# Kernel optimization log

Measured on AMD Instinct MI355X. Metric: run time of the kernel, lower is better.

The kernel has to match this reference:

```python
import jax, jax.numpy as jnp
import numpy as np

B, H, W, C = 16, 56, 56, 512
NH = 16
WS = 7
SHIFT = 3
HIDDEN = int(C * 4.0)
N = WS * WS
EPS = 1e-5


def _window_partition(x):
    # x: [B, H, W, C] -> [B*nW, N, C]
    b, h, w, c = x.shape
    x = x.reshape(b, h // WS, WS, w // WS, WS, c).transpose(0, 1, 3, 2, 4, 5)
    return x.reshape(-1, N, c)


def _window_reverse(win, h, w):
    c = win.shape[-1]
    x = win.reshape(-1, h // WS, w // WS, WS, WS, c).transpose(0, 1, 3, 2, 4, 5)
    return x.reshape(-1, h, w, c)


def _layernorm(x, g, b):
    mu = jnp.mean(x, axis=-1, keepdims=True)
    var = jnp.mean(jnp.square(x - mu), axis=-1, keepdims=True)
    return (x - mu) * jax.lax.rsqrt(var + EPS) * g + b


def _make_rel_coords_table():
    ch = np.arange(-(WS - 1), WS)
    cw = np.arange(-(WS - 1), WS)
    t = np.expand_dims(np.transpose(np.stack(np.meshgrid(ch, cw, indexing='ij')), [1, 2, 0]), 0).astype(np.float64)
    t[..., 0] /= (WS - 1)
    t[..., 1] /= (WS - 1)
    t *= 8
    t = np.sign(t) * np.log2(np.abs(t) + 1.0) / np.log2(8)
    return jnp.asarray(t, jnp.float32)  # [1, 2WS-1, 2WS-1, 2]


def _make_rel_pos_index():
    ch = np.arange(WS)
    cw = np.arange(WS)
    coords = np.reshape(np.stack(np.meshgrid(ch, cw, indexing='ij')), [2, -1])
    rel = np.expand_dims(coords, -1) - np.expand_dims(coords, -2)
    rel = np.transpose(rel, [1, 2, 0])
    rel[..., 0] += WS - 1
    rel[..., 1] += WS - 1
    rel[..., 0] *= 2 * WS - 1
    return jnp.asarray(np.sum(rel, -1), jnp.int32)  # [N, N]


def _make_attn_mask():
    img = np.zeros((H, W), np.float32)
    cnt = 0
    for hs in (slice(0, -WS), slice(-WS, -SHIFT), slice(-SHIFT, None)):
        for ws_ in (slice(0, -WS), slice(-WS, -SHIFT), slice(-SHIFT, None)):
            img[hs, ws_] = cnt
            cnt += 1
    x = img.reshape(1, H // WS, WS, W // WS, WS, 1).transpose(0, 1, 3, 2, 4, 5).reshape(-1, N)
    diff = x[:, :, None] - x[:, None, :]
    return jnp.asarray(np.where(diff != 0, -100.0, 0.0).astype(np.float32))  # [nW, N, N]


def setup_inputs() -> dict:
    key = jax.random.key(0)
    ks = jax.random.split(key, 16)
    s = 0.02
    return {
        'x': jax.random.normal(ks[0], (B, H, W, C), jnp.float32),
        'qkv_w': jax.random.normal(ks[1], (C, 3 * C), jnp.float32) * s,
        'q_bias': jnp.zeros((C,), jnp.float32),
        'v_bias': jnp.zeros((C,), jnp.float32),
        'proj_w': jax.random.normal(ks[2], (C, C), jnp.float32) * s,
        'proj_b': jnp.zeros((C,), jnp.float32),
        'logit_scale': jnp.full((NH, 1, 1), np.log(10.0), jnp.float32),
        'cpb_w1': jax.random.normal(ks[3], (2, 512), jnp.float32) * s,
        'cpb_b1': jnp.zeros((512,), jnp.float32),
        'cpb_w2': jax.random.normal(ks[4], (512, NH), jnp.float32) * s,
        'rel_coords_table': _make_rel_coords_table(),
        'gamma1': jnp.ones((C,), jnp.float32),
        'beta1': jnp.zeros((C,), jnp.float32),
        'gamma2': jnp.ones((C,), jnp.float32),
        'beta2': jnp.zeros((C,), jnp.float32),
        'fc1_w': jax.random.normal(ks[5], (C, HIDDEN), jnp.float32) * s,
        'fc1_b': jnp.zeros((HIDDEN,), jnp.float32),
        'fc2_w': jax.random.normal(ks[6], (HIDDEN, C), jnp.float32) * s,
        'fc2_b': jnp.zeros((C,), jnp.float32),
        'rel_pos_index': _make_rel_pos_index(),
        'attn_mask': _make_attn_mask(),
    }


def _forward(x, qkv_w, q_bias, v_bias, proj_w, proj_b, logit_scale,
             cpb_w1, cpb_b1, cpb_w2, rel_coords_table,
             gamma1, beta1, gamma2, beta2, fc1_w, fc1_b, fc2_w, fc2_b,
             rel_pos_index, attn_mask):
    hd = C // NH
    shortcut = x
    # cyclic shift + window partition
    xs = jnp.roll(x, (-SHIFT, -SHIFT), axis=(1, 2))
    xw = _window_partition(xs)  # [B*nW, N, C]
    # qkv with (q, 0, v) bias
    qkv_bias = jnp.concatenate([q_bias, jnp.zeros_like(v_bias), v_bias], axis=0)
    qkv = xw @ qkv_w + qkv_bias
    qkv = qkv.reshape(-1, N, 3, NH, hd).transpose(2, 0, 3, 1, 4)
    q, k, v = qkv[0], qkv[1], qkv[2]  # [BW, NH, N, hd]
    # cosine attention with learned temperature
    qn = q / jnp.linalg.norm(q, axis=-1, keepdims=True)
    kn = k / jnp.linalg.norm(k, axis=-1, keepdims=True)
    scale = jnp.exp(jnp.minimum(logit_scale, jnp.log(100.0)))
    attn = jnp.einsum('bhnd,bhmd->bhnm', qn, kn) * scale
    # continuous position bias via small MLP + gather
    cpb = jax.nn.relu(rel_coords_table @ cpb_w1 + cpb_b1) @ cpb_w2  # [1,2W-1,2W-1,NH]
    table = cpb.reshape(-1, NH)
    bias = table[rel_pos_index.reshape(-1)].reshape(N, N, NH).transpose(2, 0, 1)
    bias = 16.0 * jax.nn.sigmoid(bias)
    attn = attn + bias[None]
    # shifted-window mask
    nW = attn_mask.shape[0]
    attn = attn.reshape(-1, nW, NH, N, N) + attn_mask[None, :, None]
    attn = jax.nn.softmax(attn.reshape(-1, NH, N, N), axis=-1)
    out = jnp.einsum('bhnm,bhmd->bhnd', attn, v).transpose(0, 2, 1, 3).reshape(-1, N, C)
    out = out @ proj_w + proj_b
    # reverse windows + reverse shift
    out = _window_reverse(out, H, W)
    out = jnp.roll(out, (SHIFT, SHIFT), axis=(1, 2))
    # Swin-V2 res-post-norm residual blocks
    x1 = shortcut + _layernorm(out, gamma1, beta1)
    h = jax.nn.gelu(x1 @ fc1_w + fc1_b, approximate=False) @ fc2_w + fc2_b
    return x1 + _layernorm(h, gamma2, beta2)


def reference(x, qkv_w, q_bias, v_bias, proj_w, proj_b, logit_scale,
              cpb_w1, cpb_b1, cpb_w2, rel_coords_table,
              gamma1, beta1, gamma2, beta2, fc1_w, fc1_b, fc2_w, fc2_b,
              rel_pos_index, attn_mask):
    return _forward(x, qkv_w, q_bias, v_bias, proj_w, proj_b, logit_scale,
                    cpb_w1, cpb_b1, cpb_w2, rel_coords_table,
                    gamma1, beta1, gamma2, beta2, fc1_w, fc1_b, fc2_w, fc2_b,
                    rel_pos_index, attn_mask)
```

## Files before the change

kernel.cpp:

```cpp
#include <hip/hip_runtime.h>
#include <hip/hip_bf16.h>
#include <cmath>

typedef __hip_bfloat16 bf16;
typedef __attribute__((ext_vector_type(8))) __bf16 bf16x8;
typedef __attribute__((ext_vector_type(4))) float f32x4;
typedef __attribute__((ext_vector_type(4))) short short4v;

#define NROWS 50176

static __device__ __forceinline__ float b2f(bf16 v) { return __bfloat162float(v); }
static __device__ __forceinline__ bf16 f2b(float v) { return __float2bfloat16(v); }

static __device__ __forceinline__ void gl16(const bf16* g, bf16* l) {
  __builtin_amdgcn_global_load_lds((const __attribute__((address_space(1))) void*)g,
                                   (__attribute__((address_space(3))) void*)l, 16, 0, 0);
}

static __device__ __forceinline__ size_t pix_base(int row) {
  if (row >= NROWS) row = NROWS - 1;
  int win = row / 49, tok = row - win * 49;
  int b = win >> 6, wi = win & 63;
  int th = tok / 7, tw = tok - th * 7;
  int h = (wi >> 3) * 7 + th + 3; if (h >= 56) h -= 56;
  int w = (wi & 7) * 7 + tw + 3;  if (w >= 56) w -= 56;
  return (((size_t)b * 56 + h) * 56 + w) * 512;
}

__global__ __launch_bounds__(256) void diag_fill(float* out, float val, int n) {
  int i = blockIdx.x * 256 + threadIdx.x;
  if (i < n) out[i] = val;
}

__global__ __launch_bounds__(256) void transpose_f2b(const float* __restrict__ in,
                                                     bf16* __restrict__ out,
                                                     int R, int C) {
  __shared__ float tile[32][33];
  int c0 = blockIdx.x * 32, r0 = blockIdx.y * 32;
  int tx = threadIdx.x & 31, ty = threadIdx.x >> 5;
  for (int i = ty; i < 32; i += 8)
    tile[i][tx] = in[(size_t)(r0 + i) * C + c0 + tx];
  __syncthreads();
  for (int i = ty; i < 32; i += 8)
    out[(size_t)(c0 + i) * R + r0 + tx] = f2b(tile[tx][i]);
}

__global__ __launch_bounds__(256) void conv_f2b(const float* __restrict__ in,
                                                bf16* __restrict__ outb, int n8) {
  for (int i = blockIdx.x * 256 + threadIdx.x; i < n8; i += gridDim.x * 256) {
    float4 u0 = *(const float4*)&in[(size_t)i * 8];
    float4 u1 = *(const float4*)&in[(size_t)i * 8 + 4];
    bf16 h8[8] = {f2b(u0.x), f2b(u0.y), f2b(u0.z), f2b(u0.w),
                  f2b(u1.x), f2b(u1.y), f2b(u1.z), f2b(u1.w)};
    *(uint4*)&outb[(size_t)i * 8] = *(uint4*)h8;
  }
}

__global__ void prep_small(const float* qb, const float* vb, const float* pb,
                           const float* f1b, const float* f2b_, const float* ls,
                           float* qkvb, float* pbf, float* f1bf, float* f2bf,
                           float* scale) {
  int tid = blockIdx.x * 256 + threadIdx.x;
  if (tid < 512)       qkvb[tid] = qb[tid];
  else if (tid < 1024) qkvb[tid] = 0.f;
  else if (tid < 1536) qkvb[tid] = vb[tid - 1024];
  if (tid < 512)  pbf[tid]  = pb[tid];
  if (tid < 2048) f1bf[tid] = f1b[tid];
  if (tid < 512)  f2bf[tid] = f2b_[tid];
  if (tid < 16)   scale[tid] = expf(fminf(ls[tid], 4.6051701859880914f));
}

__global__ __launch_bounds__(256) void prep_cpb(const float* __restrict__ coords,
                                                const float* __restrict__ w1,
                                                const float* __restrict__ b1,
                                                const float* __restrict__ w2,
                                                float* __restrict__ table) {
  __shared__ float hid[512];
  __shared__ float part[256];
  int idx = blockIdx.x;
  float c0 = coords[idx * 2], c1 = coords[idx * 2 + 1];
  int tid = threadIdx.x;
  for (int h = tid; h < 512; h += 256) {
    float v = c0 * w1[h] + c1 * w1[512 + h] + b1[h];
    hid[h] = fmaxf(v, 0.f);
  }
  __syncthreads();
  int head = tid & 15, seg = tid >> 4;
  float s = 0.f;
  for (int h = seg * 32; h < seg * 32 + 32; ++h) s += hid[h] * w2[h * 16 + head];
  part[tid] = s;
  __syncthreads();
  if (tid < 16) {
    float t = 0.f;
    for (int sg = 0; sg < 16; ++sg) t += part[sg * 16 + tid];
    table[idx * 16 + tid] = t;
  }
}

__global__ void prep_bias(const float* __restrict__ table, const int* __restrict__ rpi,
                          float* __restrict__ bias_full) {
  int idx = blockIdx.x * 256 + threadIdx.x;
  if (idx >= 16 * 2401) return;
  int head = idx / 2401, ij = idx - head * 2401;
  float t = table[rpi[ij] * 16 + head];
  bias_full[idx] = 16.f / (1.f + expf(-t));
}

__global__ void prep_bm(const float* __restrict__ biasF, const float* __restrict__ amask,
                        float* __restrict__ bm) {
  int idx = blockIdx.x * 256 + threadIdx.x;
  if (idx >= 64 * 16 * 2401) return;
  int w = idx / (16 * 2401);
  int rem = idx - w * (16 * 2401);
  int h = rem / 2401, ij = rem - h * 2401;
  bm[idx] = biasF[h * 2401 + ij] + amask[w * 2401 + ij];
}

template <int EPI, int GATHER>
__global__ __launch_bounds__(256, 4) void gemm_lds(const bf16* __restrict__ A, int lda,
                                                   const bf16* __restrict__ Bt,
                                                   bf16* __restrict__ C, int ldc,
                                                   const float* __restrict__ bias,
                                                   int K, int nbx, int row_off) {
  __shared__ __align__(16) bf16 As[128 * 32];
  __shared__ __align__(16) bf16 Bs[128 * 32];
  const int nwg = gridDim.x, bid = blockIdx.x;
  const int q = nwg >> 3, r = nwg & 7;
  const int xcd = bid & 7, coff = bid >> 3;
  const int wg = (xcd < r ? xcd * (q + 1) : r * (q + 1) + (xcd - r) * q) + coff;
  const int bx = wg % nbx, by = wg / nbx;
  const int row0 = by * 128, col0 = bx * 128;

  const int tid = threadIdx.x;
  const int lane = tid & 63;
  const int quad = lane >> 4, l15 = lane & 15;
  const int wave = tid >> 6;
  const int wm = (wave >> 1) * 64, wn = (wave & 1) * 64;
  const int xq = quad ^ ((l15 >> 1) & 3);

  const int ar0 = tid >> 2, as0 = tid & 3;
  const int ar1 = ar0 + 64;
  const int ax0 = as0 ^ ((ar0 >> 1) & 3);
  const int ax1 = as0 ^ ((ar1 >> 1) & 3);
  size_t ab0, ab1;
  if (GATHER) {
    ab0 = pix_base(row_off + row0 + ar0);
    ab1 = pix_base(row_off + row0 + ar1);
  } else {
    ab0 = (size_t)(row0 + ar0) * lda;
    ab1 = (size_t)(row0 + ar1) * lda;
  }
  const bf16* ap0 = A + ab0 + ax0 * 8;
  const bf16* ap1 = A + ab1 + ax1 * 8;
  const bf16* bp0 = Bt + (size_t)(col0 + ar0) * K + ax0 * 8;
  const bf16* bp1 = Bt + (size_t)(col0 + ar1) * K + ax1 * 8;
  bf16* la0 = As + tid * 8;
  bf16* la1 = As + (tid + 256) * 8;
  bf16* lb0 = Bs + tid * 8;
  bf16* lb1 = Bs + (tid + 256) * 8;

  f32x4 acc[4][4] = {};

  for (int k0 = 0; k0 < K; k0 += 32) {
    gl16(ap0 + k0, la0);
    gl16(ap1 + k0, la1);
    gl16(bp0 + k0, lb0);
    gl16(bp1 + k0, lb1);
    __syncthreads();
    bf16x8 af[4], bfr[4];
#pragma unroll
    for (int t = 0; t < 4; ++t) {
      af[t]  = *(const bf16x8*)&As[(wm + t * 16 + l15) * 32 + xq * 8];
      bfr[t] = *(const bf16x8*)&Bs[(wn + t * 16 + l15) * 32 + xq * 8];
    }
#pragma unroll
    for (int mt = 0; mt < 4; ++mt)
#pragma unroll
      for (int nt = 0; nt < 4; ++nt)
        acc[mt][nt] = __builtin_amdgcn_mfma_f32_16x16x32_bf16(af[mt], bfr[nt], acc[mt][nt], 0, 0, 0);
    __syncthreads();
  }

#pragma unroll
  for (int nt = 0; nt < 4; ++nt) {
    int gcol = col0 + wn + nt * 16 + l15;
    float bv = bias[gcol];
#pragma unroll
    for (int mt = 0; mt < 4; ++mt) {
      int grow = row0 + wm + mt * 16 + quad * 4;
#pragma unroll
      for (int rr = 0; rr < 4; ++rr) {
        float v = acc[mt][nt][rr] + bv;
        if (EPI == 2) v = 0.5f * v * (1.0f + erff(v * 0.70710678118654752f));
        C[(size_t)(grow + rr) * ldc + gcol] = f2b(v);
      }
    }
  }
}

__global__ __launch_bounds__(256, 4) void attn_mfma(const bf16* __restrict__ qkv,
                                                    const float* __restrict__ scale,
                                                    const float* __restrict__ bm,
                                                    bf16* __restrict__ outp, int win_off) {
  __shared__ __align__(16) __bf16 Vl[4][1984];
  const int tid = threadIdx.x;
  const int wave = tid >> 6, lane = tid & 63;
  const int quad = lane >> 4, l15 = lane & 15;
  const int winl = blockIdx.x >> 2, hg = blockIdx.x & 3;
  const int head = hg * 4 + wave;
  const int wing = win_off + winl;
  const size_t rowbase = (size_t)winl * 49;
  const __bf16* base = (const __bf16*)qkv + rowbase * 1536 + head * 32;
  __bf16* Vw = Vl[wave];
  const float* bmh = bm + ((size_t)(wing & 63) * 16 + head) * 2401;
  const float sc = scale[head];

  bf16x8 vtmp[4];
  int vj[4], vdc[4];
#pragma unroll
  for (int t = 0; t < 4; ++t) {
    int c = lane + 64 * t; if (c > 195) c = 195;
    vj[t] = c >> 2; vdc[t] = (c & 3) << 3;
    vtmp[t] = *(const bf16x8*)(base + (size_t)vj[t] * 1536 + 1024 + vdc[t]);
  }

  bf16x8 khi[4], klo[4];
#pragma unroll
  for (int jt = 0; jt < 4; ++jt) {
    int j = jt * 16 + l15; if (j > 48) j = 48;
    bf16x8 raw = *(const bf16x8*)(base + (size_t)j * 1536 + 512 + quad * 8);
    float f[8]; float ss = 1e-20f;
#pragma unroll
    for (int e = 0; e < 8; ++e) { f[e] = (float)raw[e]; ss += f[e] * f[e]; }
    ss += __shfl_xor(ss, 16, 64);
    ss += __shfl_xor(ss, 32, 64);
    float inv = rsqrtf(ss);
#pragma unroll
    for (int e = 0; e < 8; ++e) {
      float v = f[e] * inv;
      __bf16 h = (__bf16)v;
      khi[jt][e] = h;
      klo[jt][e] = (__bf16)(v - (float)h);
    }
  }

#pragma unroll
  for (int t = 0; t < 4; ++t)
    *(bf16x8*)&Vw[vj[t] * 40 + vdc[t]] = vtmp[t];

  short4v vb[4][2];
#pragma unroll
  for (int jt = 0; jt < 4; ++jt)
#pragma unroll
    for (int n2 = 0; n2 < 2; ++n2) {
      short4v v;
#pragma unroll
      for (int e = 0; e < 4; ++e) {
        int j = jt * 16 + quad * 4 + e; if (j > 48) j = 48;
        v[e] = *(const short*)&Vw[j * 40 + n2 * 16 + l15];
      }
      vb[jt][n2] = v;
    }

  for (int it = 0; it < 4; ++it) {
    int qi = it * 16 + l15; if (qi > 48) qi = 48;
    bf16x8 raw = *(const bf16x8*)(base + (size_t)qi * 1536 + quad * 8);
    float f[8]; float ss = 1e-20f;
#pragma unroll
    for (int e = 0; e < 8; ++e) { f[e] = (float)raw[e]; ss += f[e] * f[e]; }
    ss += __shfl_xor(ss, 16, 64);
    ss += __shfl_xor(ss, 32, 64);
    float qinv = rsqrtf(ss) * sc;
    bf16x8 qhi, qlo;
#pragma unroll
    for (int e = 0; e < 8; ++e) {
      float v = f[e] * qinv;
      __bf16 h = (__bf16)v;
      qhi[e] = h;
      qlo[e] = (__bf16)(v - (float)h);
    }
    f32x4 s4[4];
#pragma unroll
    for (int jt = 0; jt < 4; ++jt) {
      f32x4 a = {0.f, 0.f, 0.f, 0.f};
      a = __builtin_amdgcn_mfma_f32_16x16x32_bf16(khi[jt], qhi, a, 0, 0, 0);
      a = __builtin_amdgcn_mfma_f32_16x16x32_bf16(klo[jt], qhi, a, 0, 0, 0);
      a = __builtin_amdgcn_mfma_f32_16x16x32_bf16(khi[jt], qlo, a, 0, 0, 0);
      s4[jt] = a;
    }
    int iio = qi * 49;
    float sv[4][4];
    float mx = -1e30f;
#pragma unroll
    for (int jt = 0; jt < 4; ++jt)
#pragma unroll
      for (int rr = 0; rr < 4; ++rr) {
        int j = jt * 16 + quad * 4 + rr;
        float s = (j < 49) ? s4[jt][rr] + bmh[iio + j] : -1e30f;
        sv[jt][rr] = s;
        mx = fmaxf(mx, s);
      }
    mx = fmaxf(mx, __shfl_xor(mx, 16, 64));
    mx = fmaxf(mx, __shfl_xor(mx, 32, 64));
    float sum = 0.f;
#pragma unroll
    for (int jt = 0; jt < 4; ++jt)
#pragma unroll
      for (int rr = 0; rr < 4; ++rr) {
        float e = exp2f((sv[jt][rr] - mx) * 1.4426950408889634f);
        sv[jt][rr] = e;
        sum += e;
      }
    sum += __shfl_xor(sum, 16, 64);
    sum += __shfl_xor(sum, 32, 64);
    float pinv = 1.f / sum;
    short4v pa[4];
#pragma unroll
    for (int jt = 0; jt < 4; ++jt)
#pragma unroll
      for (int rr = 0; rr < 4; ++rr) {
        __bf16 h = (__bf16)(sv[jt][rr] * pinv);
        pa[jt][rr] = *(short*)&h;
      }
    f32x4 o[2] = {};
#pragma unroll
    for (int jt = 0; jt < 4; ++jt) {
#pragma unroll
      for (int n2 = 0; n2 < 2; ++n2)
        o[n2] = __builtin_amdgcn_mfma_f32_16x16x16bf16_1k(pa[jt], vb[jt][n2], o[n2], 0, 0, 0);
    }
#pragma unroll
    for (int n2 = 0; n2 < 2; ++n2)
#pragma unroll
      for (int rr = 0; rr < 4; ++rr) {
        int i = it * 16 + quad * 4 + rr;
        if (i < 49)
          outp[(rowbase + i) * 1536 + head * 32 + n2 * 16 + l15] = f2b(o[n2][rr]);
      }
  }
}

__global__ __launch_bounds__(256) void ln_shift_add(const bf16* projq,
                                                    const float* __restrict__ x,
                                                    const float* __restrict__ gamma,
                                                    const float* __restrict__ beta,
                                                    float* __restrict__ x1,
                                                    bf16* __restrict__ x1b,
                                                    int row_off) {
  __shared__ float red[10];
  int grow = row_off + blockIdx.x;
  int win = grow / 49, tok = grow - win * 49;
  int b = win >> 6, wi = win & 63;
  int hs = (wi >> 3) * 7 + tok / 7;
  int wsc = (wi & 7) * 7 + tok % 7;
  int h = hs + 3; if (h >= 56) h -= 56;
  int w = wsc + 3; if (w >= 56) w -= 56;
  size_t pix = ((size_t)b * 56 + h) * 56 + w;
  const bf16* src = projq + (size_t)blockIdx.x * 1536 + 512;
  int tid = threadIdx.x;
  float a0 = b2f(src[tid]);
  float a1 = b2f(src[tid + 256]);
  float s = a0 + a1, qq = a0 * a0 + a1 * a1;
#pragma unroll
  for (int off = 32; off > 0; off >>= 1) {
    s += __shfl_down(s, off, 64);
    qq += __shfl_down(qq, off, 64);
  }
  int lane = tid & 63, wv = tid >> 6;
  if (lane == 0) { red[wv] = s; red[4 + wv] = qq; }
  __syncthreads();
  if (tid == 0) {
    red[8] = red[0] + red[1] + red[2] + red[3];
    red[9] = red[4] + red[5] + red[6] + red[7];
  }
  __syncthreads();
  float mu = red[8] * (1.f / 512.f);
  float inv = rsqrtf(fmaxf(red[9] * (1.f / 512.f) - mu * mu, 0.f) + 1e-5f);
  size_t base = pix * 512;
  float v0 = x[base + tid]       + (a0 - mu) * inv * gamma[tid]       + beta[tid];
  float v1 = x[base + tid + 256] + (a1 - mu) * inv * gamma[tid + 256] + beta[tid + 256];
  x1[base + tid]        = v0;
  x1[base + tid + 256]  = v1;
  x1b[base + tid]       = f2b(v0);
  x1b[base + tid + 256] = f2b(v1);
}

__global__ __launch_bounds__(256) void ln_add(const bf16* __restrict__ hsrc,
                                              float* x1,
                                              const float* __restrict__ gamma,
                                              const float* __restrict__ beta) {
  __shared__ float red[10];
  size_t base = (size_t)blockIdx.x * 512;
  int tid = threadIdx.x;
  float a0 = b2f(hsrc[base + tid]);
  float a1 = b2f(hsrc[base + tid + 256]);
  float s = a0 + a1, qq = a0 * a0 + a1 * a1;
#pragma unroll
  for (int off = 32; off > 0; off >>= 1) {
    s += __shfl_down(s, off, 64);
    qq += __shfl_down(qq, off, 64);
  }
  int lane = tid & 63, wv = tid >> 6;
  if (lane == 0) { red[wv] = s; red[4 + wv] = qq; }
  __syncthreads();
  if (tid == 0) {
    red[8] = red[0] + red[1] + red[2] + red[3];
    red[9] = red[4] + red[5] + red[6] + red[7];
  }
  __syncthreads();
  float mu = red[8] * (1.f / 512.f);
  float inv = rsqrtf(fmaxf(red[9] * (1.f / 512.f) - mu * mu, 0.f) + 1e-5f);
  x1[base + tid]       += (a0 - mu) * inv * gamma[tid]       + beta[tid];
  x1[base + tid + 256] += (a1 - mu) * inv * gamma[tid + 256] + beta[tid + 256];
}

extern "C" void kernel_launch(void* const* d_in, const int* in_sizes, int n_in,
                              void* d_out, int out_size, void* d_ws, size_t ws_size,
                              hipStream_t stream) {
  const float* x       = (const float*)d_in[0];
  const float* qkv_w   = (const float*)d_in[1];
  const float* q_bias  = (const float*)d_in[2];
  const float* v_bias  = (const float*)d_in[3];
  const float* proj_w  = (const float*)d_in[4];
  const float* proj_b  = (const float*)d_in[5];
  const float* logit_s = (const float*)d_in[6];
  const float* cpb_w1  = (const float*)d_in[7];
  const float* cpb_b1  = (const float*)d_in[8];
  const float* cpb_w2  = (const float*)d_in[9];
  const float* rct     = (const float*)d_in[10];
  const float* gamma1  = (const float*)d_in[11];
  const float* beta1   = (const float*)d_in[12];
  const float* gamma2  = (const float*)d_in[13];
  const float* beta2   = (const float*)d_in[14];
  const float* fc1_w   = (const float*)d_in[15];
  const float* fc1_b   = (const float*)d_in[16];
  const float* fc2_w   = (const float*)d_in[17];
  const float* fc2_b   = (const float*)d_in[18];
  const int*   rpi     = (const int*)d_in[19];
  const float* amask   = (const float*)d_in[20];
  float* out = (float*)d_out;

  char* ws = (char*)d_ws;
  size_t cur = 0;
  auto alloc = [&](size_t bytes) { size_t o = cur; cur += (bytes + 255) & ~(size_t)255; return o; };
  size_t o_qkvb = alloc(1536 * 4);
  size_t o_pb   = alloc(512 * 4);
  size_t o_f1b  = alloc(2048 * 4);
  size_t o_f2b  = alloc(512 * 4);
  size_t o_scal = alloc(16 * 4);
  size_t o_tab  = alloc(169 * 16 * 4);
  size_t o_bias = alloc(16 * 2401 * 4);
  size_t o_bm   = alloc((size_t)64 * 16 * 2401 * 4);
  size_t o_wt1  = alloc((size_t)1536 * 512 * 2);
  size_t o_wt2  = alloc((size_t)512 * 512 * 2);
  size_t o_wt3  = alloc((size_t)2048 * 512 * 2);
  size_t o_wt4  = alloc((size_t)512 * 2048 * 2);
  size_t o_xb   = alloc((size_t)NROWS * 512 * 2);
  size_t o_x1b  = alloc((size_t)NROWS * 512 * 2);
  size_t o_big  = cur;
  size_t avail  = (ws_size > o_big) ? ws_size - o_big : 0;

  const int wopts[] = {1024, 512, 256, 128, 64, 32, 16, 8};
  int wA = 0, padA = 0;
  for (int i = 0; i < 8; ++i) {
    int rows = wopts[i] * 49;
    int pad = (rows + 127) & ~127;
    if ((size_t)pad * 1536 * 2 <= avail) { wA = wopts[i]; padA = pad; break; }
  }
  const int ropts[] = {25088, 12544, 6272, 3584, 1792, 896, 512, 256};
  int rB = 0;
  for (int i = 0; i < 8; ++i)
    if ((size_t)ropts[i] * 2560 * 2 <= avail) { rB = ropts[i]; break; }

  if (!wA || !rB) {
    float v = 20000.f + (float)(ws_size >> 20);
    diag_fill<<<(out_size + 255) / 256, 256, 0, stream>>>(out, v, out_size);
    return;
  }

  float* qkvb  = (float*)(ws + o_qkvb);
  float* pbf   = (float*)(ws + o_pb);
  float* f1bf  = (float*)(ws + o_f1b);
  float* f2bf  = (float*)(ws + o_f2b);
  float* scal  = (float*)(ws + o_scal);
  float* tab   = (float*)(ws + o_tab);
  float* biasF = (float*)(ws + o_bias);
  float* bmF   = (float*)(ws + o_bm);
  bf16* wt1 = (bf16*)(ws + o_wt1);
  bf16* wt2 = (bf16*)(ws + o_wt2);
  bf16* wt3 = (bf16*)(ws + o_wt3);
  bf16* wt4 = (bf16*)(ws + o_wt4);
  bf16* xb  = (bf16*)(ws + o_xb);
  bf16* x1b = (bf16*)(ws + o_x1b);
  bf16* big = (bf16*)(ws + o_big);

  transpose_f2b<<<dim3(48, 16), 256, 0, stream>>>(qkv_w, wt1, 512, 1536);
  transpose_f2b<<<dim3(16, 16), 256, 0, stream>>>(proj_w, wt2, 512, 512);
  transpose_f2b<<<dim3(64, 16), 256, 0, stream>>>(fc1_w, wt3, 512, 2048);
  transpose_f2b<<<dim3(16, 64), 256, 0, stream>>>(fc2_w, wt4, 2048, 512);
  conv_f2b<<<2048, 256, 0, stream>>>(x, xb, NROWS * 512 / 8);

  prep_small<<<8, 256, 0, stream>>>(q_bias, v_bias, proj_b, fc1_b, fc2_b, logit_s,
                                    qkvb, pbf, f1bf, f2bf, scal);
  prep_cpb<<<169, 256, 0, stream>>>(rct, cpb_w1, cpb_b1, cpb_w2, tab);
  prep_bias<<<151, 256, 0, stream>>>(tab, rpi, biasF);
  prep_bm<<<(64 * 16 * 2401 + 255) / 256, 256, 0, stream>>>(biasF, amask, bmF);

  for (int woff = 0; woff < 1024; woff += wA) {
    int row_off = woff * 49;
    int rows = wA * 49;
    int nby = padA / 128;
    bf16* qkvC = big;
    gemm_lds<1, 1><<<12 * nby, 256, 0, stream>>>(xb, 0, wt1, qkvC, 1536, qkvb, 512, 12, row_off);
    attn_mfma<<<wA * 4, 256, 0, stream>>>(qkvC, scal, bmF, qkvC, woff);
    gemm_lds<1, 0><<<4 * nby, 256, 0, stream>>>(qkvC, 1536, wt2, qkvC + 512, 1536, pbf, 512, 4, 0);
    ln_shift_add<<<rows, 256, 0, stream>>>(qkvC, x, gamma1, beta1, out, x1b, row_off);
  }
  for (int r0 = 0; r0 < NROWS; r0 += rB) {
    float* x1h = out + (size_t)r0 * 512;
    bf16* hC  = big;
    bf16* f2C = big + (size_t)rB * 2048;
    int nby = rB / 128;
    gemm_lds<2, 0><<<16 * nby, 256, 0, stream>>>(x1b + (size_t)r0 * 512, 512, wt3, hC, 2048, f1bf, 512, 16, 0);
    gemm_lds<1, 0><<<4 * nby, 256, 0, stream>>>(hC, 2048, wt4, f2C, 512, f2bf, 2048, 4, 0);
    ln_add<<<rB, 256, 0, stream>>>(f2C, x1h, gamma2, beta2);
  }
}
```

Measured before the change: 958.0 us.

## Triple-buffer GEMM K-loop, stage epilogue through LDS, use fast GELU approximation

Replaces the single-buffered GEMM K-loop with a 3-stage global_load_lds pipeline that uses explicit vmcnt waits, so loads for the next tiles overlap with the MFMA work on the current one. The epilogue now writes results to an LDS tile and then stores 16-byte coalesced rows, instead of scattered 2-byte global stores. GELU uses an Abramowitz-Stegun erf polynomial with rcp/exp2 in place of erff. The change raises LDS use to 48KB and lowers the occupancy hint to 3 blocks per CU, and the erf approximation adds a small numerical error.

```diff
diff --git a/kernel.cpp b/kernel.cpp
--- a/kernel.cpp
+++ b/kernel.cpp
@@ -15,6 +15,17 @@
 static __device__ __forceinline__ void gl16(const bf16* g, bf16* l) {
   __builtin_amdgcn_global_load_lds((const __attribute__((address_space(1))) void*)g,
                                    (__attribute__((address_space(3))) void*)l, 16, 0, 0);
+}
+
+static __device__ __forceinline__ float fast_gelu(float v) {
+  float z = v * 0.70710678118654752f;
+  float a = fabsf(z);
+  float t = __builtin_amdgcn_rcpf(fmaf(0.3275911f, a, 1.0f));
+  float poly = t * fmaf(t, fmaf(t, fmaf(t, fmaf(t, 1.061405429f, -1.453152027f),
+                                        1.421413741f), -0.284496736f), 0.254829592f);
+  float e = exp2f(-a * a * 1.4426950408889634f);
+  float erfz = copysignf(1.0f - poly * e, z);
+  return 0.5f * v * (1.0f + erfz);
 }
 
 static __device__ __forceinline__ size_t pix_base(int row) {
@@ -117,13 +128,14 @@
 }
 
 template <int EPI, int GATHER>
-__global__ __launch_bounds__(256, 4) void gemm_lds(const bf16* __restrict__ A, int lda,
+__global__ __launch_bounds__(256, 3) void gemm_lds(const bf16* __restrict__ A, int lda,
                                                    const bf16* __restrict__ Bt,
                                                    bf16* __restrict__ C, int ldc,
                                                    const float* __restrict__ bias,
                                                    int K, int nbx, int row_off) {
-  __shared__ __align__(16) bf16 As[128 * 32];
-  __shared__ __align__(16) bf16 Bs[128 * 32];
+  __shared__ __align__(16) char smem[49152];
+  bf16* Ct = (bf16*)smem;
+
   const int nwg = gridDim.x, bid = blockIdx.x;
   const int q = nwg >> 3, r = nwg & 7;
   const int xcd = bid & 7, coff = bid >> 3;
@@ -154,47 +166,77 @@
   const bf16* ap1 = A + ab1 + ax1 * 8;
   const bf16* bp0 = Bt + (size_t)(col0 + ar0) * K + ax0 * 8;
   const bf16* bp1 = Bt + (size_t)(col0 + ar1) * K + ax1 * 8;
-  bf16* la0 = As + tid * 8;
-  bf16* la1 = As + (tid + 256) * 8;
-  bf16* lb0 = Bs + tid * 8;
-  bf16* lb1 = Bs + (tid + 256) * 8;
 
   f32x4 acc[4][4] = {};
-
-  for (int k0 = 0; k0 < K; k0 += 32) {
-    gl16(ap0 + k0, la0);
-    gl16(ap1 + k0, la1);
-    gl16(bp0 + k0, lb0);
-    gl16(bp1 + k0, lb1);
-    __syncthreads();
-    bf16x8 af[4], bfr[4];
-#pragma unroll
-    for (int t = 0; t < 4; ++t) {
-      af[t]  = *(const bf16x8*)&As[(wm + t * 16 + l15) * 32 + xq * 8];
-      bfr[t] = *(const bf16x8*)&Bs[(wn + t * 16 + l15) * 32 + xq * 8];
-    }
-#pragma unroll
-    for (int mt = 0; mt < 4; ++mt)
-#pragma unroll
-      for (int nt = 0; nt < 4; ++nt)
-        acc[mt][nt] = __builtin_amdgcn_mfma_f32_16x16x32_bf16(af[mt], bfr[nt], acc[mt][nt], 0, 0, 0);
-    __syncthreads();
-  }
+  const int NK = K >> 5;
+
+#define BUF_A(s) ((bf16*)(smem + (s) * 16384))
+#define BUF_B(s) ((bf16*)(smem + (s) * 16384 + 8192))
+#define STAGE(s, KK)                              \
+  do {                                            \
+    gl16(ap0 + (KK), BUF_A(s) + tid * 8);         \
+    gl16(ap1 + (KK), BUF_A(s) + (tid + 256) * 8); \
+    gl16(bp0 + (KK), BUF_B(s) + tid * 8);         \
+    gl16(bp1 + (KK), BUF_B(s) + (tid + 256) * 8); \
+  } while (0)
+
+  STAGE(0, 0);
+  STAGE(1, 32);
+  STAGE(2, 64);
+
+  int s = 0;
+  for (int kt = 0; kt < NK; ++kt) {
+    if (kt + 2 < NK)      asm volatile("s_waitcnt vmcnt(8)" ::: "memory");
+    else if (kt + 1 < NK) asm volatile("s_waitcnt vmcnt(4)" ::: "memory");
+    else                  asm volatile("s_waitcnt vmcnt(0)" ::: "memory");
+    __builtin_amdgcn_sched_barrier(0);
+    __builtin_amdgcn_s_barrier();
+    __builtin_amdgcn_sched_barrier(0);
+    {
+      bf16x8 af[4], bfr[4];
+#pragma unroll
+      for (int t = 0; t < 4; ++t) {
+        af[t]  = *(const bf16x8*)&BUF_A(s)[(wm + t * 16 + l15) * 32 + xq * 8];
+        bfr[t] = *(const bf16x8*)&BUF_B(s)[(wn + t * 16 + l15) * 32 + xq * 8];
+      }
+#pragma unroll
+      for (int mt = 0; mt < 4; ++mt)
+#pragma unroll
+        for (int nt = 0; nt < 4; ++nt)
+          acc[mt][nt] = __builtin_amdgcn_mfma_f32_16x16x32_bf16(af[mt], bfr[nt], acc[mt][nt], 0, 0, 0);
+    }
+    __builtin_amdgcn_sched_barrier(0);
+    __builtin_amdgcn_s_barrier();
+    __builtin_amdgcn_sched_barrier(0);
+    if (kt + 3 < NK) STAGE(s, (kt + 3) * 32);
+    s = (s == 2) ? 0 : s + 1;
+  }
+#undef STAGE
+#undef BUF_A
+#undef BUF_B
 
 #pragma unroll
   for (int nt = 0; nt < 4; ++nt) {
-    int gcol = col0 + wn + nt * 16 + l15;
-    float bv = bias[gcol];
+    int lcol = wn + nt * 16 + l15;
+    float bv = bias[col0 + lcol];
 #pragma unroll
     for (int mt = 0; mt < 4; ++mt) {
-      int grow = row0 + wm + mt * 16 + quad * 4;
+      int lrow = wm + mt * 16 + quad * 4;
 #pragma unroll
       for (int rr = 0; rr < 4; ++rr) {
         float v = acc[mt][nt][rr] + bv;
-        if (EPI == 2) v = 0.5f * v * (1.0f + erff(v * 0.70710678118654752f));
-        C[(size_t)(grow + rr) * ldc + gcol] = f2b(v);
-      }
-    }
+        if (EPI == 2) v = fast_gelu(v);
+        Ct[(lrow + rr) * 136 + lcol] = f2b(v);
+      }
+    }
+  }
+  __syncthreads();
+#pragma unroll
+  for (int i = 0; i < 8; ++i) {
+    int chunk = tid + i * 256;
+    int rw = chunk >> 4, c16 = chunk & 15;
+    uint4 val = *(const uint4*)&Ct[rw * 136 + c16 * 8];
+    *(uint4*)&C[(size_t)(row0 + rw) * ldc + col0 + c16 * 8] = val;
   }
 }
 
```

Measured after the change: 890.1 us. 1.08x faster.
